# Kernel tuning notes

Measured on AMD Instinct MI355X. Metric: run time of the kernel, lower is better.

## Reference

```python
import jax, jax.numpy as jnp
import numpy as np


def setup_inputs() -> dict:
    key = jax.random.key(0)
    kq, kk, kv, kmask = jax.random.split(key, 4)
    B, H, L, D = 2, 16, 2048, 64
    q = jax.random.normal(kq, (B, H, L, D), dtype=jnp.float32)
    k = jax.random.normal(kk, (B, H, L, D), dtype=jnp.float32)
    v = jax.random.normal(kv, (B, H, L, D), dtype=jnp.float32)
    valid = jax.random.randint(kmask, (B, H, L, L), 0, 2, dtype=jnp.int32)
    scale = jnp.ones((), dtype=jnp.float32)  # typically 1/sqrt(D)
    return {"q": q, "k": k, "v": v, "valid": valid, "scale": scale}


def reference(q, k, v, valid, scale):
    # scores: [B, H, Lq, Lk]
    att_v = jnp.einsum('bhqd,bhkd->bhqk', q, k)
    att_v = att_v * scale
    att_v = att_v - jnp.max(att_v, axis=-1, keepdims=True)
    att_v = jnp.where(valid <= 0, -jnp.inf, att_v)
    att_w = jax.nn.softmax(att_v, axis=-1)
    # rows that are fully masked produce NaN -> zero them (matches torch masked_fill on isnan)
    att_w = jnp.where(jnp.isnan(att_w), jnp.zeros((), dtype=att_w.dtype), att_w)
    result = jnp.einsum('bhqk,bhkd->bhqd', att_w, v)
    return (result, att_w)
```

## Files before the change

### kernel.cpp

```cpp
#include <hip/hip_runtime.h>
#include <hip/hip_fp16.h>

#define L_    2048
#define D_    64
#define QT    64
#define NKT   32
#define KP16  72
#define VTP   72
#define PBP   72

typedef _Float16 half8  __attribute__((ext_vector_type(8)));
typedef _Float16 half4  __attribute__((ext_vector_type(4)));
typedef _Float16 half2v __attribute__((ext_vector_type(2)));
typedef float    f32x4  __attribute__((ext_vector_type(4)));

__device__ __forceinline__ f32x4 mfma16f(half8 a, half8 b, f32x4 c) {
    return __builtin_amdgcn_mfma_f32_16x16x32_f16(a, b, c, 0, 0, 0);
}

#define FENCE_BAR() do { asm volatile("s_waitcnt lgkmcnt(0)" ::: "memory"); \
                         __builtin_amdgcn_s_barrier();                       \
                         asm volatile("" ::: "memory"); } while (0)

__global__ __launch_bounds__(256, 4)
void attn_fused(const float* __restrict__ Qg, const float* __restrict__ Kg,
                const float* __restrict__ Vg, const int* __restrict__ validg,
                const float* __restrict__ scaleg,
                float* __restrict__ outR, float* __restrict__ outW)
{
    __shared__ __attribute__((aligned(16))) _Float16 Klds[64 * KP16];
    __shared__ __attribute__((aligned(16))) _Float16 Vt[64 * VTP];
    __shared__ __attribute__((aligned(16))) _Float16 Pbuf[64 * PBP];

    const int tid  = threadIdx.x;
    const int wv   = tid >> 6;
    const int lane = tid & 63;
    const int ln   = lane & 15;
    const int qd   = lane >> 4;

    const int bidx = blockIdx.x;
    const int bh   = (bidx & 7) * 4 + ((bidx >> 3) & 3);
    const int qt   = bidx >> 5;

    const float scale = scaleg[0];

    const float* Qb = Qg + ((size_t)bh * L_ + (size_t)qt * QT) * D_;
    const float* Kb = Kg + (size_t)bh * L_ * D_;
    const float* Vb = Vg + (size_t)bh * L_ * D_;
    const int*   Mb = validg + ((size_t)bh * L_ + (size_t)qt * QT) * (size_t)L_;
    float* Ob = outR + ((size_t)bh * L_ + (size_t)qt * QT) * D_;
    float* Wb = outW + ((size_t)bh * L_ + (size_t)qt * QT) * (size_t)L_;

    half8 aF[2];
    {
        const float* qrow = Qb + (size_t)(wv * 16 + ln) * D_;
#pragma unroll
        for (int f = 0; f < 2; ++f) {
            f32x4 x0 = *(const f32x4*)(qrow + f * 32 + qd * 8);
            f32x4 x1 = *(const f32x4*)(qrow + f * 32 + qd * 8 + 4);
            half8 h;
#pragma unroll
            for (int j = 0; j < 4; ++j) { h[j] = (_Float16)x0[j]; h[4 + j] = (_Float16)x1[j]; }
            aF[f] = h;
        }
    }

    f32x4 kreg[4];
    const int kt4 = tid >> 4;
    const int kc4 = (tid & 15) * 4;
    auto loadK = [&](int kt) {
        const float* base = Kb + (size_t)kt * (64 * 64);
#pragma unroll
        for (int j = 0; j < 4; ++j)
            kreg[j] = *(const f32x4*)(base + (size_t)(j * 256 + tid) * 4);
    };
    auto writeK = [&]() {
#pragma unroll
        for (int j = 0; j < 4; ++j) {
            const int row = j * 16 + kt4;
            half4 h;
#pragma unroll
            for (int e = 0; e < 4; ++e) h[e] = (_Float16)kreg[j][e];
            *(half4*)&Klds[row * KP16 + kc4] = h;
        }
    };

    f32x4 vreg[4];
    const int rp = tid >> 3;
    const int vc = tid & 7;
    const int dc = vc * 8;
    auto loadV = [&](int kt) {
        const float* v0p = Vb + ((size_t)kt * 64 + 2 * rp) * 64 + dc;
        vreg[0] = *(const f32x4*)v0p;
        vreg[1] = *(const f32x4*)(v0p + 4);
        vreg[2] = *(const f32x4*)(v0p + 64);
        vreg[3] = *(const f32x4*)(v0p + 68);
    };
    auto writeV = [&]() {
        const int g = (rp >> 2) ^ vc;
#pragma unroll
        for (int i = 0; i < 8; ++i) {
            float f0 = (i < 4) ? vreg[0][i] : vreg[1][i - 4];
            float f1 = (i < 4) ? vreg[2][i] : vreg[3][i - 4];
            half2v h; h[0] = (_Float16)f0; h[1] = (_Float16)f1;
            const int d = dc + i;
            *(half2v*)&Vt[d * VTP + 8 * g + 2 * (rp & 3)] = h;
        }
    };

    int mv[16];
    const int* maskbase = Mb + (size_t)(wv * 16 + qd * 4) * L_ + ln;
    auto loadM = [&](int kt) {
#pragma unroll
        for (int ct = 0; ct < 4; ++ct)
#pragma unroll
            for (int r = 0; r < 4; ++r)
                mv[ct * 4 + r] = maskbase[(size_t)r * L_ + kt * 64 + ct * 16];
    };

    auto kfrags = [&](int kr, half8& b0, half8& b1) {
        const _Float16* kp = &Klds[kr * KP16 + qd * 8];
        b0 = *(const half8*)kp;
        b1 = *(const half8*)(kp + 32);
    };

    unsigned short* bitsSlab = (unsigned short*)Ob;

    float lsum[4] = {0.f, 0.f, 0.f, 0.f};
    loadK(0); loadM(0);
    for (int kt = 0; kt < NKT; ++kt) {
        FENCE_BAR();
        writeK();
        unsigned bits = 0;
#pragma unroll
        for (int i = 0; i < 16; ++i) bits |= (mv[i] > 0 ? 1u : 0u) << i;
        if (kt + 1 < NKT) { loadK(kt + 1); loadM(kt + 1); }
        FENCE_BAR();
        bitsSlab[kt * 256 + tid] = (unsigned short)bits;
#pragma unroll
        for (int ct = 0; ct < 4; ++ct) {
            half8 b0, b1;
            kfrags(ct * 16 + ln, b0, b1);
            f32x4 acc = {0.f, 0.f, 0.f, 0.f};
            acc = mfma16f(aF[0], b0, acc);
            acc = mfma16f(aF[1], b1, acc);
#pragma unroll
            for (int r = 0; r < 4; ++r) {
                float bit = (float)((bits >> (ct * 4 + r)) & 1u);
                lsum[r] += bit * __expf(acc[r] * scale);
            }
        }
    }

    float invl[4];
#pragma unroll
    for (int r = 0; r < 4; ++r) {
        float v = lsum[r];
        v += __shfl_xor(v, 1);
        v += __shfl_xor(v, 2);
        v += __shfl_xor(v, 4);
        v += __shfl_xor(v, 8);
        invl[r] = v > 0.f ? 1.f / v : 0.f;
    }

    asm volatile("s_waitcnt vmcnt(0)" ::: "memory");

    f32x4 accO[4];
#pragma unroll
    for (int i = 0; i < 4; ++i) accO[i] = (f32x4){0.f, 0.f, 0.f, 0.f};

    loadK(0); loadV(0);
    unsigned bcur = bitsSlab[tid];
    for (int kt = 0; kt < NKT; ++kt) {
        FENCE_BAR();
        writeK();
        writeV();
        unsigned bnext = 0;
        if (kt + 1 < NKT) {
            loadK(kt + 1); loadV(kt + 1);
            bnext = bitsSlab[(kt + 1) * 256 + tid];
        }
        FENCE_BAR();
        const unsigned bits = bcur;
#pragma unroll
        for (int ct = 0; ct < 4; ++ct) {
            half8 b0, b1;
            kfrags(ct * 16 + ln, b0, b1);
            f32x4 acc = {0.f, 0.f, 0.f, 0.f};
            acc = mfma16f(aF[0], b0, acc);
            acc = mfma16f(aF[1], b1, acc);
#pragma unroll
            for (int r = 0; r < 4; ++r) {
                const int qrow = wv * 16 + qd * 4 + r;
                float bit = (float)((bits >> (ct * 4 + r)) & 1u);
                float p = bit * __expf(acc[r] * scale) * invl[r];
                Pbuf[qrow * PBP + ct * 16 + ln] = (_Float16)p;
            }
        }
        half8 p0 = *(const half8*)&Pbuf[(wv * 16 + ln) * PBP + qd * 8];
        half8 p1 = *(const half8*)&Pbuf[(wv * 16 + ln) * PBP + 32 + qd * 8];
        {
            float* wp = Wb + (size_t)(wv * 16 + ln) * L_ + kt * 64;
            f32x4 s0, s1, s2, s3;
#pragma unroll
            for (int j = 0; j < 4; ++j) {
                s0[j] = (float)p0[j];     s1[j] = (float)p0[4 + j];
                s2[j] = (float)p1[j];     s3[j] = (float)p1[4 + j];
            }
            *(f32x4*)(wp + qd * 8)          = s0;
            *(f32x4*)(wp + qd * 8 + 4)      = s1;
            *(f32x4*)(wp + 32 + qd * 8)     = s2;
            *(f32x4*)(wp + 32 + qd * 8 + 4) = s3;
        }
#pragma unroll
        for (int c2 = 0; c2 < 4; ++c2) {
            const int d  = c2 * 16 + ln;
            const int g2 = (d >> 3) & 7;
            half8 v0 = *(const half8*)&Vt[d * VTP + 8 * (qd ^ g2)];
            half8 v1 = *(const half8*)&Vt[d * VTP + 8 * ((4 + qd) ^ g2)];
            accO[c2] = mfma16f(p0, v0, accO[c2]);
            accO[c2] = mfma16f(p1, v1, accO[c2]);
        }
        bcur = bnext;
    }

#pragma unroll
    for (int c2 = 0; c2 < 4; ++c2)
#pragma unroll
        for (int r = 0; r < 4; ++r)
            Ob[(size_t)(wv * 16 + qd * 4 + r) * D_ + (c2 * 16 + ln)] = accO[c2][r];
}

extern "C" void kernel_launch(void* const* d_in, const int* in_sizes, int n_in,
                              void* d_out, int out_size, void* d_ws, size_t ws_size,
                              hipStream_t stream) {
    const float* q     = (const float*)d_in[0];
    const float* k     = (const float*)d_in[1];
    const float* v     = (const float*)d_in[2];
    const int*   valid = (const int*)d_in[3];
    const float* scale = (const float*)d_in[4];

    float* out_res  = (float*)d_out;
    float* out_attw = out_res + (size_t)2 * 16 * L_ * D_;

    dim3 grid(2 * 16 * (L_ / QT));
    dim3 block(256);
    attn_fused<<<grid, block, 0, stream>>>(q, k, v, valid, scale, out_res, out_attw);
}
```

Measured before the change: 1.095 ms.

## Pre-convert K and transpose V to fp16 in workspace, drop LDS staging

```diff
diff --git a/kernel.cpp b/kernel.cpp
--- a/kernel.cpp
+++ b/kernel.cpp
@@ -5,31 +5,68 @@
 #define D_    64
 #define QT    64
 #define NKT   32
-#define KP16  72
-#define VTP   72
 #define PBP   72
 
 typedef _Float16 half8  __attribute__((ext_vector_type(8)));
 typedef _Float16 half4  __attribute__((ext_vector_type(4)));
-typedef _Float16 half2v __attribute__((ext_vector_type(2)));
 typedef float    f32x4  __attribute__((ext_vector_type(4)));
 
 __device__ __forceinline__ f32x4 mfma16f(half8 a, half8 b, f32x4 c) {
     return __builtin_amdgcn_mfma_f32_16x16x32_f16(a, b, c, 0, 0, 0);
 }
 
-#define FENCE_BAR() do { asm volatile("s_waitcnt lgkmcnt(0)" ::: "memory"); \
-                         __builtin_amdgcn_s_barrier();                       \
-                         asm volatile("" ::: "memory"); } while (0)
-
+__global__ __launch_bounds__(256)
+void cvt_k(const float* __restrict__ Kg, _Float16* __restrict__ Kh)
+{
+    const int base = blockIdx.x * 1024 + threadIdx.x;
+#pragma unroll
+    for (int j = 0; j < 4; ++j) {
+        const size_t c = (size_t)base + (size_t)j * 256;
+        f32x4 x = ((const f32x4*)Kg)[c];
+        half4 h;
+#pragma unroll
+        for (int e = 0; e < 4; ++e) h[e] = (_Float16)x[e];
+        ((half4*)Kh)[c] = h;
+    }
+}
+
+__global__ __launch_bounds__(256)
+void tr_v(const float* __restrict__ Vg, _Float16* __restrict__ Vth)
+{
+    __shared__ float t[64][65];
+    const int bh = blockIdx.x >> 5;
+    const int kt = blockIdx.x & 31;
+    const float* src = Vg + ((size_t)bh * L_ + (size_t)kt * 64) * D_;
+    const int tid = threadIdx.x;
+#pragma unroll
+    for (int j = 0; j < 4; ++j) {
+        const int k = j * 16 + (tid >> 4);
+        const int d = (tid & 15) * 4;
+        f32x4 x = *(const f32x4*)(src + k * 64 + d);
+#pragma unroll
+        for (int e = 0; e < 4; ++e) t[d + e][k] = x[e];
+    }
+    __syncthreads();
+    _Float16* dst = Vth + (size_t)bh * 64 * L_ + (size_t)kt * 64;
+#pragma unroll
+    for (int j = 0; j < 4; ++j) {
+        const int d = j * 16 + (tid >> 4);
+        const int k = (tid & 15) * 4;
+        half4 h;
+#pragma unroll
+        for (int e = 0; e < 4; ++e) h[e] = (_Float16)t[d][k + e];
+        *(half4*)(dst + (size_t)d * L_ + k) = h;
+    }
+}
+
+template<bool WS>
 __global__ __launch_bounds__(256, 4)
 void attn_fused(const float* __restrict__ Qg, const float* __restrict__ Kg,
                 const float* __restrict__ Vg, const int* __restrict__ validg,
                 const float* __restrict__ scaleg,
+                const _Float16* __restrict__ Khg, const _Float16* __restrict__ Vthg,
                 float* __restrict__ outR, float* __restrict__ outW)
 {
-    __shared__ __attribute__((aligned(16))) _Float16 Klds[64 * KP16];
-    __shared__ __attribute__((aligned(16))) _Float16 Vt[64 * VTP];
     __shared__ __attribute__((aligned(16))) _Float16 Pbuf[64 * PBP];
 
     const int tid  = threadIdx.x;
@@ -47,6 +84,8 @@
     const float* Qb = Qg + ((size_t)bh * L_ + (size_t)qt * QT) * D_;
     const float* Kb = Kg + (size_t)bh * L_ * D_;
     const float* Vb = Vg + (size_t)bh * L_ * D_;
+    const _Float16* Khb  = Khg  ? Khg  + (size_t)bh * L_ * D_ : nullptr;
+    const _Float16* Vthb = Vthg ? Vthg + (size_t)bh * D_ * L_ : nullptr;
     const int*   Mb = validg + ((size_t)bh * L_ + (size_t)qt * QT) * (size_t)L_;
     float* Ob = outR + ((size_t)bh * L_ + (size_t)qt * QT) * D_;
     float* Wb = outW + ((size_t)bh * L_ + (size_t)qt * QT) * (size_t)L_;
@@ -65,46 +104,37 @@
         }
     }
 
-    f32x4 kreg[4];
-    const int kt4 = tid >> 4;
-    const int kc4 = (tid & 15) * 4;
-    auto loadK = [&](int kt) {
-        const float* base = Kb + (size_t)kt * (64 * 64);
-#pragma unroll
-        for (int j = 0; j < 4; ++j)
-            kreg[j] = *(const f32x4*)(base + (size_t)(j * 256 + tid) * 4);
+    auto kfrag = [&](int kt, int ct, half8& b0, half8& b1) {
+        if constexpr (WS) {
+            const _Float16* p = Khb + (size_t)(kt * 64 + ct * 16 + ln) * D_ + qd * 8;
+            b0 = *(const half8*)p;
+            b1 = *(const half8*)(p + 32);
+        } else {
+            const float* p = Kb + (size_t)(kt * 64 + ct * 16 + ln) * D_ + qd * 8;
+            f32x4 x0 = *(const f32x4*)p;
+            f32x4 x1 = *(const f32x4*)(p + 4);
+            f32x4 y0 = *(const f32x4*)(p + 32);
+            f32x4 y1 = *(const f32x4*)(p + 36);
+#pragma unroll
+            for (int j = 0; j < 4; ++j) {
+                b0[j] = (_Float16)x0[j]; b0[4 + j] = (_Float16)x1[j];
+                b1[j] = (_Float16)y0[j]; b1[4 + j] = (_Float16)y1[j];
+            }
+        }
     };
-    auto writeK = [&]() {
-#pragma unroll
-        for (int j = 0; j < 4; ++j) {
-            const int row = j * 16 + kt4;
-            half4 h;
-#pragma unroll
-            for (int e = 0; e < 4; ++e) h[e] = (_Float16)kreg[j][e];
-            *(half4*)&Klds[row * KP16 + kc4] = h;
-        }
-    };
-
-    f32x4 vreg[4];
-    const int rp = tid >> 3;
-    const int vc = tid & 7;
-    const int dc = vc * 8;
-    auto loadV = [&](int kt) {
-        const float* v0p = Vb + ((size_t)kt * 64 + 2 * rp) * 64 + dc;
-        vreg[0] = *(const f32x4*)v0p;
-        vreg[1] = *(const f32x4*)(v0p + 4);
-        vreg[2] = *(const f32x4*)(v0p + 64);
-        vreg[3] = *(const f32x4*)(v0p + 68);
-    };
-    auto writeV = [&]() {
-        const int g = (rp >> 2) ^ vc;
-#pragma unroll
-        for (int i = 0; i < 8; ++i) {
-            float f0 = (i < 4) ? vreg[0][i] : vreg[1][i - 4];
-            float f1 = (i < 4) ? vreg[2][i] : vreg[3][i - 4];
-            half2v h; h[0] = (_Float16)f0; h[1] = (_Float16)f1;
-            const int d = dc + i;
-            *(half2v*)&Vt[d * VTP + 8 * g + 2 * (rp & 3)] = h;
+
+    auto vfrag = [&](int kt, int c2, half8& v0, half8& v1) {
+        if constexpr (WS) {
+            const _Float16* p = Vthb + (size_t)(c2 * 16 + ln) * L_ + kt * 64 + qd * 8;
+            v0 = *(const half8*)p;
+            v1 = *(const half8*)(p + 32);
+        } else {
+            const float* p = Vb + (size_t)(kt * 64 + qd * 8) * D_ + (c2 * 16 + ln);
+#pragma unroll
+            for (int j = 0; j < 8; ++j) v0[j] = (_Float16)p[j * 64];
+            p += 32 * 64;
+#pragma unroll
+            for (int j = 0; j < 8; ++j) v1[j] = (_Float16)p[j * 64];
         }
     };
 
@@ -118,32 +148,24 @@
                 mv[ct * 4 + r] = maskbase[(size_t)r * L_ + kt * 64 + ct * 16];
     };
 
-    auto kfrags = [&](int kr, half8& b0, half8& b1) {
-        const _Float16* kp = &Klds[kr * KP16 + qd * 8];
-        b0 = *(const half8*)kp;
-        b1 = *(const half8*)(kp + 32);
-    };
-
     unsigned short* bitsSlab = (unsigned short*)Ob;
 
     float lsum[4] = {0.f, 0.f, 0.f, 0.f};
-    loadK(0); loadM(0);
+    loadM(0);
     for (int kt = 0; kt < NKT; ++kt) {
-        FENCE_BAR();
-        writeK();
+        half8 kb[4][2];
+#pragma unroll
+        for (int ct = 0; ct < 4; ++ct) kfrag(kt, ct, kb[ct][0], kb[ct][1]);
         unsigned bits = 0;
 #pragma unroll
         for (int i = 0; i < 16; ++i) bits |= (mv[i] > 0 ? 1u : 0u) << i;
-        if (kt + 1 < NKT) { loadK(kt + 1); loadM(kt + 1); }
-        FENCE_BAR();
+        if (kt + 1 < NKT) loadM(kt + 1);
         bitsSlab[kt * 256 + tid] = (unsigned short)bits;
 #pragma unroll
         for (int ct = 0; ct < 4; ++ct) {
-            half8 b0, b1;
-            kfrags(ct * 16 + ln, b0, b1);
             f32x4 acc = {0.f, 0.f, 0.f, 0.f};
-            acc = mfma16f(aF[0], b0, acc);
-            acc = mfma16f(aF[1], b1, acc);
+            acc = mfma16f(aF[0], kb[ct][0], acc);
+            acc = mfma16f(aF[1], kb[ct][1], acc);
 #pragma unroll
             for (int r = 0; r < 4; ++r) {
                 float bit = (float)((bits >> (ct * 4 + r)) & 1u);
@@ -169,23 +191,14 @@
 #pragma unroll
     for (int i = 0; i < 4; ++i) accO[i] = (f32x4){0.f, 0.f, 0.f, 0.f};
 
-    loadK(0); loadV(0);
     unsigned bcur = bitsSlab[tid];
     for (int kt = 0; kt < NKT; ++kt) {
-        FENCE_BAR();
-        writeK();
-        writeV();
-        unsigned bnext = 0;
-        if (kt + 1 < NKT) {
-            loadK(kt + 1); loadV(kt + 1);
-            bnext = bitsSlab[(kt + 1) * 256 + tid];
-        }
-        FENCE_BAR();
+        unsigned bnext = (kt + 1 < NKT) ? (unsigned)bitsSlab[(kt + 1) * 256 + tid] : 0u;
         const unsigned bits = bcur;
 #pragma unroll
         for (int ct = 0; ct < 4; ++ct) {
             half8 b0, b1;
-            kfrags(ct * 16 + ln, b0, b1);
+            kfrag(kt, ct, b0, b1);
             f32x4 acc = {0.f, 0.f, 0.f, 0.f};
             acc = mfma16f(aF[0], b0, acc);
             acc = mfma16f(aF[1], b1, acc);
@@ -214,15 +227,15 @@
         }
 #pragma unroll
         for (int c2 = 0; c2 < 4; ++c2) {
-            const int d  = c2 * 16 + ln;
-            const int g2 = (d >> 3) & 7;
-            half8 v0 = *(const half8*)&Vt[d * VTP + 8 * (qd ^ g2)];
-            half8 v1 = *(const half8*)&Vt[d * VTP + 8 * ((4 + qd) ^ g2)];
+            half8 v0, v1;
+            vfrag(kt, c2, v0, v1);
             accO[c2] = mfma16f(p0, v0, accO[c2]);
             accO[c2] = mfma16f(p1, v1, accO[c2]);
         }
         bcur = bnext;
     }
+
+    __syncthreads();
 
 #pragma unroll
     for (int c2 = 0; c2 < 4; ++c2)
@@ -243,7 +256,21 @@
     float* out_res  = (float*)d_out;
     float* out_attw = out_res + (size_t)2 * 16 * L_ * D_;
 
+    const size_t elems = (size_t)2 * 16 * L_ * D_;
+    const size_t need  = 2 * elems * sizeof(_Float16);
+
     dim3 grid(2 * 16 * (L_ / QT));
     dim3 block(256);
-    attn_fused<<<grid, block, 0, stream>>>(q, k, v, valid, scale, out_res, out_attw);
-}
+
+    if (ws_size >= need && d_ws != nullptr) {
+        _Float16* Kh  = (_Float16*)d_ws;
+        _Float16* Vth = Kh + elems;
+        cvt_k<<<dim3(1024), dim3(256), 0, stream>>>(k, Kh);
+        tr_v <<<dim3(1024), dim3(256), 0, stream>>>(v, Vth);
+        attn_fused<true><<<grid, block, 0, stream>>>(q, k, v, valid, scale, Kh, Vth,
+                                                     out_res, out_attw);
+    } else {
+        attn_fused<false><<<grid, block, 0, stream>>>(q, k, v, valid, scale, nullptr, nullptr,
+                                                      out_res, out_attw);
+    }
+}
```

Result: slower. 1.238 ms (+13.0%).
